# Kernel tuning notes

Measured on AMD Instinct MI355X. Metric: run time of the kernel, lower is better.

Reference implementation:

```python
import jax, jax.numpy as jnp
import numpy as np

B, S = 4, 128
N_ITERS = 3  # original hardcodes range(3) regardless of max_iter


def _build_masks(edge_mask, chart_mask):
    S_ = edge_mask.shape[-1]
    ar = jnp.arange(S_)
    ne = ar[:, None] != ar[None, :]          # [a,b]: a != b
    le = ar[:, None] <= ar[None, :]
    ge = ar[:, None] >= ar[None, :]
    ls = jnp.minimum(ar[:, None], ar[None, :])  # min(a,b)
    rs = jnp.maximum(ar[:, None], ar[None, :])  # max(a,b)

    # edge_mask2o[b,h,m,s] = edge_mask[b,h,s] & edge_mask[b,h,m] & (m != s)
    em2o = edge_mask[:, :, None, :] & edge_mask[:, :, :, None]
    em2o = em2o & ne[None, None, :, :]
    # lrhs[h,m,s] = (min(m,s) >= h) | (max(m,s) <= h)
    lrhs = (ls[None, :, :] >= ar[:, None, None]) | (rs[None, :, :] <= ar[:, None, None])
    noncross = em2o & lrhs[None]
    # additionally require h != s for plain edge_mask2o
    em2o = em2o & ne[:, None, :][None]

    cm0 = chart_mask[:, 0]                                  # [B,S]
    pad = cm0[:, :, None] & cm0[:, None, :]                 # [B,S,S]
    chart_r = jnp.roll(chart_mask, 1, axis=1)               # cat((cm[:,-1:], cm[:,:-1]))
    # span_mask2o[b,i,j,s] = chart_r[b,i,j] & pad[b,j,s] & (max(i,j) != s)
    span2o = chart_r[:, :, :, None] & pad[:, None, :, :]
    span2o = span2o & (rs[:, :, None] != ar[None, None, :])[None]
    # inside[i,j,s] = (i <= s) & (j >= s)
    inside = le[:, None, :] & ge[None, :, :]
    outside = (~inside)[None] & span2o
    # off-diagonal pad mask: pad.triu(1) | pad.tril(-1) == pad & (i != j)
    outside = outside & (pad & ne[None])[:, :, :, None]
    return em2o, noncross, span2o, outside


def setup_inputs() -> dict:
    key = jax.random.key(0)
    ks = jax.random.split(key, 12)
    lens = jax.random.randint(ks[0], (B,), S // 2, S)
    valid = jnp.arange(S)[None, :] < lens[:, None]          # [B,S]
    edge_mask = valid[:, :, None] & valid[:, None, :]
    tri = jnp.triu(jnp.ones((S, S), dtype=bool), 1)
    chart_mask = edge_mask & tri[None]
    def rn(k, shape):
        return jax.random.normal(k, shape, dtype=jnp.float32)
    return {
        's_edge': rn(ks[1], (B, S, S)),
        's_const': rn(ks[2], (B, S, S)),
        's_sib': rn(ks[3], (B, S, S, S)),
        's_cop': rn(ks[4], (B, S, S, S)),
        's_grd': rn(ks[5], (B, S, S, S)),
        's_end_point': rn(ks[6], (B, S, S, S)),
        's_split': rn(ks[7], (B, S, S, S)),
        's_head_span_b': rn(ks[8], (B, S, S, S)),
        's_head_span_e': rn(ks[9], (B, S, S, S)),
        'edge_mask': edge_mask,
        'chart_mask': chart_mask,
    }


def reference(s_edge, s_const, s_sib, s_cop, s_grd, s_end_point, s_split,
              s_head_span_b, s_head_span_e, edge_mask, chart_mask):
    # symmetrize span scores: triu + triu(1).T on last two dims
    s_span = jnp.triu(s_const) + jnp.swapaxes(jnp.triu(s_const, 1), -1, -2)
    em2o, noncross, span2o, outside = _build_masks(edge_mask, chart_mask)

    s_sib = s_sib * em2o
    s_cop = s_cop * em2o
    s_grd = s_grd * em2o
    s_end_point = s_end_point * noncross
    s_split = s_split * span2o
    s_hb = s_head_span_b * outside
    s_he = jnp.transpose(s_head_span_e, (0, 2, 1, 3)) * outside

    # Note: the torch code aliases tmp_q_edge to s_edge and uses +=, so the
    # base scores accumulate across iterations; equivalently q <- q + update.
    q_edge, q_span = s_edge, s_span
    for _ in range(N_ITERS):
        pe = jax.nn.sigmoid(q_edge)
        ps = jax.nn.sigmoid(q_span)
        upd_e = (jnp.einsum('bhs,bhms->bhm', pe, s_sib)
                 + jnp.einsum('bsm,bhms->bhm', pe, s_cop)
                 + jnp.einsum('bms,bhms->bhm', ps, s_grd)
                 + jnp.einsum('bms,bhms->bhm', ps, s_end_point))
        upd_s = (jnp.einsum('bis,bijs->bis', ps, s_split)
                 + jnp.einsum('bsi,bijs->bij', pe, s_hb)
                 + jnp.einsum('bsj,bijs->bij', pe, s_he))
        q_edge = q_edge + upd_e
        q_span = q_span + upd_s
    return q_edge, q_span
```

## Files before the change

### kernel.cpp

```cpp
#include <hip/hip_runtime.h>
#include <stdint.h>

#define BB 4
#define SDIM 128
#define S2 (SDIM*SDIM)
#define S3 ((size_t)SDIM*S2)

__device__ __forceinline__ int probe_len(const void* em, int b, int lane) {
    const unsigned char* p8 = (const unsigned char*)em;
    const int* p32 = (const int*)em;
    const int t0 = lane, t1 = lane + 64;
    const size_t i0 = (size_t)b*S2 + (size_t)t0*SDIM + t0;
    const size_t i1 = (size_t)b*S2 + (size_t)t1*SDIM + t1;
    const unsigned char a0 = p8[i0], a1 = p8[i1];
    const bool ok = (a0 != 0) && (t1 != SDIM-1 || a1 == 0);
    const unsigned long long mok = __ballot(ok);
    const bool use8 = (mok == ~0ull);
    int v0, v1;
    if (use8) { v0 = (a0 != 0); v1 = (a1 != 0); }
    else      { v0 = (p32[i0] != 0); v1 = (p32[i1] != 0); }
    return __popcll(__ballot(v0)) + __popcll(__ballot(v1));
}

__device__ __forceinline__ float sigf(float x) { return 1.f / (1.f + expf(-x)); }

__device__ __forceinline__ void gll16(const float* g, float* l) {
    __builtin_amdgcn_global_load_lds(
        (const __attribute__((address_space(1))) void*)g,
        (__attribute__((address_space(3))) void*)l, 16, 0, 0);
}

__global__ __launch_bounds__(256) void k_prep(
    const float* __restrict__ s_edge, const float* __restrict__ s_const,
    const float* __restrict__ s_split, const void* __restrict__ em,
    float* __restrict__ q_edge, float* __restrict__ q_span,
    float* __restrict__ split0, float* __restrict__ split1,
    float* __restrict__ peA, float* __restrict__ peB,
    float* __restrict__ peTA, float* __restrict__ peTB,
    float* __restrict__ psA, float* __restrict__ psB) {
    __shared__ float plds[64*SDIM];
    __shared__ float red2[2][SDIM];
    const int b = blockIdx.x >> 7, i = blockIdx.x & 127;
    const int y = blockIdx.y;
    const int tid = threadIdx.x, lane = tid & 63, wave = tid >> 6;
    const int len = probe_len(em, b, lane);
    const int lm1 = len - 1;
    const size_t vb = (size_t)b*S2;
    if (y == 0 && tid < SDIM) {
        const size_t ro = vb + (size_t)i*SDIM + tid;
        const float qe = s_edge[ro];
        const float qs = (i <= tid) ? s_const[ro] : s_const[vb + (size_t)tid*SDIM + i];
        q_edge[ro] = qe;
        q_span[ro] = qs;
        const float se = sigf(qe), ss = sigf(qs);
        peA[ro] = se; peB[ro] = se;
        psA[ro] = ss; psB[ro] = ss;
        const size_t to = vb + (size_t)tid*SDIM + i;
        peTA[to] = se; peTB[to] = se;
    }
    if (i >= 1 && i < len) {
        const int L = len - i;
        const float* sb = s_split + (size_t)b*S3 + (size_t)i*S2;
        for (int mloc = wave; mloc < 32; mloc += 4) {
            const int t0 = 2*(y + 2*mloc);
            if (t0 >= L) break;
            const int j = i + t0 + (lane >> 5);
            const int jc = min(j, lm1);
            gll16(sb + (size_t)jc*SDIM + (lane & 31)*4, &plds[(2*mloc)*SDIM]);
        }
    }
    __syncthreads();
    const int k = tid & 127, rh = tid >> 7;
    float sum = 0.f;
    #pragma unroll
    for (int u = 0; u < 32; ++u) {
        const int r = rh + 2*u;
        const int j = i + 4*u + 2*y + rh;
        sum += (j < len && j != k) ? plds[r*SDIM + k] : 0.f;
    }
    red2[rh][k] = sum;
    __syncthreads();
    if (tid < SDIM) {
        float* out = y ? split1 : split0;
        out[vb + (size_t)i*SDIM + tid] =
            (i >= 1 && i < len && tid >= 1 && tid < len)
            ? (red2[0][tid] + red2[1][tid]) : 0.f;
    }
}

__global__ __launch_bounds__(256) void k_upd(
    const float* __restrict__ s_sib, const float* __restrict__ s_cop,
    const float* __restrict__ s_grd, const float* __restrict__ s_ep,
    const float* __restrict__ s_hb,  const float* __restrict__ s_he,
    const float* __restrict__ peA, const float* __restrict__ peTA,
    const float* __restrict__ psA,
    const float* __restrict__ split0, const float* __restrict__ split1,
    const void* __restrict__ em,
    float* __restrict__ q_edge, float* __restrict__ q_span,
    float* __restrict__ peB, float* __restrict__ peTB, float* __restrict__ psB) {
    __shared__ float lds[6*16*SDIM];
    __shared__ float sml[64];
    const int b = blockIdx.x >> 7, row = blockIdx.x & 127;
    const int tid = threadIdx.x, wave = tid >> 6, lane = tid & 63;
    const int half = lane >> 5, sq = (lane & 31) * 4;
    const int len = probe_len(em, b, lane);
    const int lm1 = len - 1;
    const size_t vb = (size_t)b*S2;

    if (blockIdx.y < 8) {
        const int h = row;
        const int m0 = blockIdx.y * 16;
        if (h >= len || m0 >= len) return;
        const size_t tb = (size_t)b*S3 + (size_t)h*S2;
        const size_t hrow = vb + (size_t)h*SDIM;
        const float* bases[6] = { s_sib + tb, s_cop + tb, s_grd + tb,
                                  s_ep + tb,  peTA + vb,  psA + vb };
        #pragma unroll
        for (int T = 0; T < 6; ++T) {
            #pragma unroll
            for (int ss = 0; ss < 2; ++ss) {
                const int s  = 2*wave + ss;
                const int r2 = 2*s + half;
                const int mc = min(m0 + r2, lm1);
                gll16(bases[T] + (size_t)mc*SDIM + sq, &lds[(T*16 + 2*s)*SDIM]);
            }
        }
        if (tid < 16)
            sml[tid] = q_edge[hrow + min(m0 + tid, lm1)];
        __syncthreads();
        const float4 pe4 = *(const float4*)(peA + hrow + sq);
        #pragma unroll
        for (int it = 0; it < 2; ++it) {
            const int m = m0 + it*8 + wave*2 + half;
            const int r = it*8 + wave*2 + half;
            const float4 sibv = *(const float4*)&lds[(0*16 + r)*SDIM + sq];
            const float4 copv = *(const float4*)&lds[(1*16 + r)*SDIM + sq];
            const float4 grdv = *(const float4*)&lds[(2*16 + r)*SDIM + sq];
            const float4 epvv = *(const float4*)&lds[(3*16 + r)*SDIM + sq];
            const float4 petv = *(const float4*)&lds[(4*16 + r)*SDIM + sq];
            const float4 psvv = *(const float4*)&lds[(5*16 + r)*SDIM + sq];
            const bool mv = (m < len);
            float rr = 0.f;
            #define TERM(C, F) { const int s = sq + C;                               \
                const bool bs = mv && (s < len) && (m != s);                         \
                const float fem = (bs && (h != s)) ? 1.f : 0.f;                      \
                const float fnc = (bs && ((m >= h && s >= h) || (m <= h && s <= h))) \
                                  ? 1.f : 0.f;                                       \
                rr += fem * (sibv.F*pe4.F + copv.F*petv.F + grdv.F*psvv.F)           \
                    + fnc * (epvv.F*psvv.F); }
            TERM(0, x) TERM(1, y) TERM(2, z) TERM(3, w)
            #undef TERM
            rr += __shfl_xor(rr, 16); rr += __shfl_xor(rr, 8); rr += __shfl_xor(rr, 4);
            rr += __shfl_xor(rr, 2);  rr += __shfl_xor(rr, 1);
            if ((lane & 31) == 0 && mv) {
                const float qn = sml[r] + rr;
                q_edge[hrow + m] = qn;
                const float sg = sigf(qn);
                peB[hrow + m] = sg;
                peTB[vb + (size_t)m*SDIM + h] = sg;
            }
        }
    } else {
        const int i = row;
        const int j0 = (blockIdx.y - 8) * 16;
        if (i < 1 || i >= len || j0 >= len) return;
        const size_t irow = vb + (size_t)i*SDIM;
        #pragma unroll
        for (int ss = 0; ss < 2; ++ss) {
            const int s  = 2*wave + ss;
            const int r2 = 2*s + half;
            const int jc = min(j0 + r2, lm1);
            gll16(s_hb + (size_t)b*S3 + (size_t)i*S2 + (size_t)jc*SDIM + sq,
                  &lds[(0*16 + 2*s)*SDIM]);
            gll16(s_he + (size_t)b*S3 + (size_t)jc*S2 + (size_t)i*SDIM + sq,
                  &lds[(1*16 + 2*s)*SDIM]);
            gll16(peTA + vb + (size_t)jc*SDIM + sq,
                  &lds[(2*16 + 2*s)*SDIM]);
        }
        if (tid < 64) {
            const int surf = tid >> 4, jj = tid & 15;
            const int jc = min(j0 + jj, lm1);
            const size_t o = irow + jc;
            const float v = (surf == 0) ? q_span[o]
                          : (surf == 1) ? psA[o]
                          : (surf == 2) ? split0[o] : split1[o];
            sml[tid] = v;
        }
        __syncthreads();
        const float4 peTi4 = *(const float4*)(peTA + irow + sq);
        #pragma unroll
        for (int it = 0; it < 2; ++it) {
            const int j = j0 + it*8 + wave*2 + half;
            const int r = it*8 + wave*2 + half;
            const float4 hbv  = *(const float4*)&lds[(0*16 + r)*SDIM + sq];
            const float4 hev  = *(const float4*)&lds[(1*16 + r)*SDIM + sq];
            const float4 ptjv = *(const float4*)&lds[(2*16 + r)*SDIM + sq];
            const bool act = (j > i) && (j < len);
            float rr = 0.f;
            #define TERM(C, F) { const int s = sq + C;                               \
                const float f = (act && s >= 1 && s < len && (s < i || s > j))       \
                                ? 1.f : 0.f;                                         \
                rr += f * (hbv.F*peTi4.F + hev.F*ptjv.F); }
            TERM(0, x) TERM(1, y) TERM(2, z) TERM(3, w)
            #undef TERM
            rr += __shfl_xor(rr, 16); rr += __shfl_xor(rr, 8); rr += __shfl_xor(rr, 4);
            rr += __shfl_xor(rr, 2);  rr += __shfl_xor(rr, 1);
            if ((lane & 31) == 0 && j >= 1 && j < len) {
                const float qn = sml[r] + rr + sml[16 + r] * (sml[32 + r] + sml[48 + r]);
                q_span[irow + j] = qn;
                psB[irow + j] = sigf(qn);
            }
        }
    }
}

extern "C" void kernel_launch(void* const* d_in, const int* in_sizes, int n_in,
                              void* d_out, int out_size, void* d_ws, size_t ws_size,
                              hipStream_t stream) {
    const float* s_edge  = (const float*)d_in[0];
    const float* s_const = (const float*)d_in[1];
    const float* s_sib   = (const float*)d_in[2];
    const float* s_cop   = (const float*)d_in[3];
    const float* s_grd   = (const float*)d_in[4];
    const float* s_ep    = (const float*)d_in[5];
    const float* s_split = (const float*)d_in[6];
    const float* s_hb    = (const float*)d_in[7];
    const float* s_he    = (const float*)d_in[8];
    const void*  em      = d_in[9];
    (void)in_sizes; (void)n_in; (void)out_size; (void)ws_size;

    float* q_edge = (float*)d_out;
    float* q_span = q_edge + (size_t)BB * S2;

    char* ws = (char*)d_ws;
    const size_t SZ = (size_t)BB * S2 * sizeof(float);
    float* split0 = (float*)(ws);
    float* split1 = (float*)(ws + 1*SZ);
    float* peA    = (float*)(ws + 2*SZ);
    float* peTA   = (float*)(ws + 3*SZ);
    float* psA    = (float*)(ws + 4*SZ);
    float* peB    = (float*)(ws + 5*SZ);
    float* peTB   = (float*)(ws + 6*SZ);
    float* psB    = (float*)(ws + 7*SZ);

    const int NB = BB * SDIM;
    hipLaunchKernelGGL(k_prep, dim3(NB, 2), dim3(256), 0, stream,
                       s_edge, s_const, s_split, em, q_edge, q_span,
                       split0, split1, peA, peB, peTA, peTB, psA, psB);
    for (int it = 0; it < 3; ++it) {
        const int s = it & 1;
        const float* peR  = s ? peB  : peA;
        const float* peTR = s ? peTB : peTA;
        const float* psR  = s ? psB  : psA;
        float* peW  = s ? peA  : peB;
        float* peTW = s ? peTA : peTB;
        float* psW  = s ? psA  : psB;
        hipLaunchKernelGGL(k_upd, dim3(dim3(NB, 16)), dim3(256), 0, stream,
                           s_sib, s_cop, s_grd, s_ep, s_hb, s_he,
                           peR, peTR, psR, split0, split1, em,
                           q_edge, q_span, peW, peTW, psW);
    }
}
```

Baseline: 294.6 us.

## Restructure update kernels into per-row persistent blocks with double-buffered async loads

The grid changes from many 16-row tiles per (batch,row) to one block per row and part. Each block loops over 8-row chunks and double-buffers global-to-LDS loads, using explicit vmcnt waits so the next chunk's fetch overlaps compute on the current one. The split prep kernel is collapsed into a single pass that writes one summed split buffer, and span rows below the diagonal skip the tensor loads entirely. This trades grid-level parallelism (fewer, longer blocks) for less redundant row-header loading and better latency hiding, with the risk of lower occupancy and load imbalance across rows of different lengths.

```diff
diff --git a/kernel.cpp b/kernel.cpp
--- a/kernel.cpp
+++ b/kernel.cpp
@@ -34,19 +34,18 @@
     const float* __restrict__ s_edge, const float* __restrict__ s_const,
     const float* __restrict__ s_split, const void* __restrict__ em,
     float* __restrict__ q_edge, float* __restrict__ q_span,
-    float* __restrict__ split0, float* __restrict__ split1,
+    float* __restrict__ splitsum,
     float* __restrict__ peA, float* __restrict__ peB,
     float* __restrict__ peTA, float* __restrict__ peTB,
     float* __restrict__ psA, float* __restrict__ psB) {
-    __shared__ float plds[64*SDIM];
-    __shared__ float red2[2][SDIM];
+    __shared__ float pbuf[2][8][SDIM];
+    __shared__ float pred[2][SDIM];
     const int b = blockIdx.x >> 7, i = blockIdx.x & 127;
-    const int y = blockIdx.y;
-    const int tid = threadIdx.x, lane = tid & 63, wave = tid >> 6;
+    const int tid = threadIdx.x, lane = tid & 63, wave = tid >> 6, half = lane >> 5;
     const int len = probe_len(em, b, lane);
     const int lm1 = len - 1;
     const size_t vb = (size_t)b*S2;
-    if (y == 0 && tid < SDIM) {
+    if (tid < SDIM) {
         const size_t ro = vb + (size_t)i*SDIM + tid;
         const float qe = s_edge[ro];
         const float qs = (i <= tid) ? s_const[ro] : s_const[vb + (size_t)tid*SDIM + i];
@@ -58,34 +57,42 @@
         const size_t to = vb + (size_t)tid*SDIM + i;
         peTA[to] = se; peTB[to] = se;
     }
+    float sumv = 0.f;
     if (i >= 1 && i < len) {
-        const int L = len - i;
         const float* sb = s_split + (size_t)b*S3 + (size_t)i*S2;
-        for (int mloc = wave; mloc < 32; mloc += 4) {
-            const int t0 = 2*(y + 2*mloc);
-            if (t0 >= L) break;
-            const int j = i + t0 + (lane >> 5);
-            const int jc = min(j, lm1);
-            gll16(sb + (size_t)jc*SDIM + (lane & 31)*4, &plds[(2*mloc)*SDIM]);
-        }
-    }
-    __syncthreads();
-    const int k = tid & 127, rh = tid >> 7;
-    float sum = 0.f;
-    #pragma unroll
-    for (int u = 0; u < 32; ++u) {
-        const int r = rh + 2*u;
-        const int j = i + 4*u + 2*y + rh;
-        sum += (j < len && j != k) ? plds[r*SDIM + k] : 0.f;
-    }
-    red2[rh][k] = sum;
-    __syncthreads();
-    if (tid < SDIM) {
-        float* out = y ? split1 : split0;
-        out[vb + (size_t)i*SDIM + tid] =
-            (i >= 1 && i < len && tid >= 1 && tid < len)
-            ? (red2[0][tid] + red2[1][tid]) : 0.f;
-    }
+        const int sq = (lane & 31) * 4;
+        const int nc = (len - i + 7) >> 3;
+        #define PSTAGE(CB, C) { \
+            const int jc_ = min(i + 8*(C) + 2*wave + half, lm1); \
+            gll16(sb + (size_t)jc_*SDIM + sq, &pbuf[CB][2*wave][0]); }
+        PSTAGE(0, 0)
+        const int k = tid & 127, rh = tid >> 7;
+        float acc = 0.f;
+        for (int c = 0; c < nc; ++c) {
+            const int cb = c & 1;
+            if (c + 1 < nc) {
+                PSTAGE(cb ^ 1, c + 1)
+                asm volatile("s_waitcnt vmcnt(1)" ::: "memory");
+            } else {
+                asm volatile("s_waitcnt vmcnt(0)" ::: "memory");
+            }
+            __builtin_amdgcn_s_barrier();
+            #pragma unroll
+            for (int rr2 = 0; rr2 < 4; ++rr2) {
+                const int r = rh*4 + rr2;
+                const int j = i + 8*c + r;
+                const float v = pbuf[cb][r][k];
+                acc += (j < len && j != k) ? v : 0.f;
+            }
+            __builtin_amdgcn_s_barrier();
+        }
+        #undef PSTAGE
+        pred[rh][k] = acc;
+        __syncthreads();
+        if (tid >= 1 && tid < len && tid < SDIM)
+            sumv = pred[0][tid] + pred[1][tid];
+    }
+    if (tid < SDIM) splitsum[vb + (size_t)i*SDIM + tid] = sumv;
 }
 
 __global__ __launch_bounds__(256) void k_upd(
@@ -93,53 +100,57 @@
     const float* __restrict__ s_grd, const float* __restrict__ s_ep,
     const float* __restrict__ s_hb,  const float* __restrict__ s_he,
     const float* __restrict__ peA, const float* __restrict__ peTA,
-    const float* __restrict__ psA,
-    const float* __restrict__ split0, const float* __restrict__ split1,
+    const float* __restrict__ psA, const float* __restrict__ splitsum,
     const void* __restrict__ em,
     float* __restrict__ q_edge, float* __restrict__ q_span,
     float* __restrict__ peB, float* __restrict__ peTB, float* __restrict__ psB) {
-    __shared__ float lds[6*16*SDIM];
-    __shared__ float sml[64];
-    const int b = blockIdx.x >> 7, row = blockIdx.x & 127;
+    __shared__ float buf[2][6][8][SDIM];
+    __shared__ float sml[3*SDIM];
+    const int gid = blockIdx.x;
+    const int part = gid & 1, b = (gid >> 1) & 3, row = gid >> 3;
     const int tid = threadIdx.x, wave = tid >> 6, lane = tid & 63;
     const int half = lane >> 5, sq = (lane & 31) * 4;
     const int len = probe_len(em, b, lane);
     const int lm1 = len - 1;
     const size_t vb = (size_t)b*S2;
 
-    if (blockIdx.y < 8) {
+    if (part == 0) {
         const int h = row;
-        const int m0 = blockIdx.y * 16;
-        if (h >= len || m0 >= len) return;
+        if (h >= len) return;
         const size_t tb = (size_t)b*S3 + (size_t)h*S2;
         const size_t hrow = vb + (size_t)h*SDIM;
-        const float* bases[6] = { s_sib + tb, s_cop + tb, s_grd + tb,
-                                  s_ep + tb,  peTA + vb,  psA + vb };
-        #pragma unroll
-        for (int T = 0; T < 6; ++T) {
-            #pragma unroll
-            for (int ss = 0; ss < 2; ++ss) {
-                const int s  = 2*wave + ss;
-                const int r2 = 2*s + half;
-                const int mc = min(m0 + r2, lm1);
-                gll16(bases[T] + (size_t)mc*SDIM + sq, &lds[(T*16 + 2*s)*SDIM]);
-            }
-        }
-        if (tid < 16)
-            sml[tid] = q_edge[hrow + min(m0 + tid, lm1)];
+        const float4 pe4 = *(const float4*)(peA + hrow + sq);
+        if (tid < SDIM) sml[tid] = q_edge[hrow + tid];
         __syncthreads();
-        const float4 pe4 = *(const float4*)(peA + hrow + sq);
-        #pragma unroll
-        for (int it = 0; it < 2; ++it) {
-            const int m = m0 + it*8 + wave*2 + half;
-            const int r = it*8 + wave*2 + half;
-            const float4 sibv = *(const float4*)&lds[(0*16 + r)*SDIM + sq];
-            const float4 copv = *(const float4*)&lds[(1*16 + r)*SDIM + sq];
-            const float4 grdv = *(const float4*)&lds[(2*16 + r)*SDIM + sq];
-            const float4 epvv = *(const float4*)&lds[(3*16 + r)*SDIM + sq];
-            const float4 petv = *(const float4*)&lds[(4*16 + r)*SDIM + sq];
-            const float4 psvv = *(const float4*)&lds[(5*16 + r)*SDIM + sq];
+        const int nc = (len + 7) >> 3;
+        #define ESTAGE(CB, C) { \
+            const int mc_ = min(8*(C) + 2*wave + half, lm1); \
+            const size_t go = (size_t)mc_*SDIM + sq; \
+            gll16(s_sib + tb + go, &buf[CB][0][2*wave][0]); \
+            gll16(s_cop + tb + go, &buf[CB][1][2*wave][0]); \
+            gll16(s_grd + tb + go, &buf[CB][2][2*wave][0]); \
+            gll16(s_ep  + tb + go, &buf[CB][3][2*wave][0]); \
+            gll16(peTA + vb + go, &buf[CB][4][2*wave][0]); \
+            gll16(psA  + vb + go, &buf[CB][5][2*wave][0]); }
+        ESTAGE(0, 0)
+        for (int c = 0; c < nc; ++c) {
+            const int cb = c & 1;
+            if (c + 1 < nc) {
+                ESTAGE(cb ^ 1, c + 1)
+                asm volatile("s_waitcnt vmcnt(6)" ::: "memory");
+            } else {
+                asm volatile("s_waitcnt vmcnt(0)" ::: "memory");
+            }
+            __builtin_amdgcn_s_barrier();
+            const int r = 2*wave + half;
+            const int m = 8*c + r;
             const bool mv = (m < len);
+            const float4 sibv = *(const float4*)&buf[cb][0][r][sq];
+            const float4 copv = *(const float4*)&buf[cb][1][r][sq];
+            const float4 grdv = *(const float4*)&buf[cb][2][r][sq];
+            const float4 epvv = *(const float4*)&buf[cb][3][r][sq];
+            const float4 petv = *(const float4*)&buf[cb][4][r][sq];
+            const float4 psvv = *(const float4*)&buf[cb][5][r][sq];
             float rr = 0.f;
             #define TERM(C, F) { const int s = sq + C;                               \
                 const bool bs = mv && (s < len) && (m != s);                         \
@@ -153,63 +164,76 @@
             rr += __shfl_xor(rr, 16); rr += __shfl_xor(rr, 8); rr += __shfl_xor(rr, 4);
             rr += __shfl_xor(rr, 2);  rr += __shfl_xor(rr, 1);
             if ((lane & 31) == 0 && mv) {
-                const float qn = sml[r] + rr;
+                const float qn = sml[m] + rr;
                 q_edge[hrow + m] = qn;
                 const float sg = sigf(qn);
                 peB[hrow + m] = sg;
                 peTB[vb + (size_t)m*SDIM + h] = sg;
             }
-        }
+            __builtin_amdgcn_s_barrier();
+        }
+        #undef ESTAGE
     } else {
         const int i = row;
-        const int j0 = (blockIdx.y - 8) * 16;
-        if (i < 1 || i >= len || j0 >= len) return;
+        if (i < 1 || i >= len) return;
         const size_t irow = vb + (size_t)i*SDIM;
-        #pragma unroll
-        for (int ss = 0; ss < 2; ++ss) {
-            const int s  = 2*wave + ss;
-            const int r2 = 2*s + half;
-            const int jc = min(j0 + r2, lm1);
-            gll16(s_hb + (size_t)b*S3 + (size_t)i*S2 + (size_t)jc*SDIM + sq,
-                  &lds[(0*16 + 2*s)*SDIM]);
-            gll16(s_he + (size_t)b*S3 + (size_t)jc*S2 + (size_t)i*SDIM + sq,
-                  &lds[(1*16 + 2*s)*SDIM]);
-            gll16(peTA + vb + (size_t)jc*SDIM + sq,
-                  &lds[(2*16 + 2*s)*SDIM]);
-        }
-        if (tid < 64) {
-            const int surf = tid >> 4, jj = tid & 15;
-            const int jc = min(j0 + jj, lm1);
-            const size_t o = irow + jc;
-            const float v = (surf == 0) ? q_span[o]
-                          : (surf == 1) ? psA[o]
-                          : (surf == 2) ? split0[o] : split1[o];
-            sml[tid] = v;
+        const size_t ibase = (size_t)b*S3 + (size_t)i*S2;
+        const float4 peTi4 = *(const float4*)(peTA + irow + sq);
+        for (int u = tid; u < 3*SDIM; u += 256) {
+            const int surf = u >> 7, t2 = u & 127;
+            sml[u] = (surf == 0) ? q_span[irow + t2]
+                   : (surf == 1) ? psA[irow + t2] : splitsum[irow + t2];
         }
         __syncthreads();
-        const float4 peTi4 = *(const float4*)(peTA + irow + sq);
-        #pragma unroll
-        for (int it = 0; it < 2; ++it) {
-            const int j = j0 + it*8 + wave*2 + half;
-            const int r = it*8 + wave*2 + half;
-            const float4 hbv  = *(const float4*)&lds[(0*16 + r)*SDIM + sq];
-            const float4 hev  = *(const float4*)&lds[(1*16 + r)*SDIM + sq];
-            const float4 ptjv = *(const float4*)&lds[(2*16 + r)*SDIM + sq];
-            const bool act = (j > i) && (j < len);
-            float rr = 0.f;
-            #define TERM(C, F) { const int s = sq + C;                               \
-                const float f = (act && s >= 1 && s < len && (s < i || s > j))       \
-                                ? 1.f : 0.f;                                         \
-                rr += f * (hbv.F*peTi4.F + hev.F*ptjv.F); }
-            TERM(0, x) TERM(1, y) TERM(2, z) TERM(3, w)
-            #undef TERM
-            rr += __shfl_xor(rr, 16); rr += __shfl_xor(rr, 8); rr += __shfl_xor(rr, 4);
-            rr += __shfl_xor(rr, 2);  rr += __shfl_xor(rr, 1);
-            if ((lane & 31) == 0 && j >= 1 && j < len) {
-                const float qn = sml[r] + rr + sml[16 + r] * (sml[32 + r] + sml[48 + r]);
-                q_span[irow + j] = qn;
-                psB[irow + j] = sigf(qn);
-            }
+        const int c0 = (i + 1) >> 3;
+        const int nc = (len + 7) >> 3;
+        for (int j2 = tid; j2 < 8*c0; j2 += 256) {
+            if (j2 >= 1) {
+                const float qn = sml[j2] + sml[SDIM + j2] * sml[2*SDIM + j2];
+                q_span[irow + j2] = qn;
+                psB[irow + j2] = sigf(qn);
+            }
+        }
+        if (c0 < nc) {
+            #define SSTAGE(CB, C) { \
+                const int jc_ = min(8*(C) + 2*wave + half, lm1); \
+                gll16(s_hb + ibase + (size_t)jc_*SDIM + sq, &buf[CB][0][2*wave][0]); \
+                gll16(s_he + (size_t)b*S3 + (size_t)jc_*S2 + (size_t)i*SDIM + sq, \
+                      &buf[CB][1][2*wave][0]); \
+                gll16(peTA + vb + (size_t)jc_*SDIM + sq, &buf[CB][2][2*wave][0]); }
+            SSTAGE(0, c0)
+            for (int c = c0; c < nc; ++c) {
+                const int cb = (c - c0) & 1;
+                if (c + 1 < nc) {
+                    SSTAGE(cb ^ 1, c + 1)
+                    asm volatile("s_waitcnt vmcnt(3)" ::: "memory");
+                } else {
+                    asm volatile("s_waitcnt vmcnt(0)" ::: "memory");
+                }
+                __builtin_amdgcn_s_barrier();
+                const int r = 2*wave + half;
+                const int j = 8*c + r;
+                const bool act = (j > i) && (j < len);
+                const float4 hbv  = *(const float4*)&buf[cb][0][r][sq];
+                const float4 hev  = *(const float4*)&buf[cb][1][r][sq];
+                const float4 ptjv = *(const float4*)&buf[cb][2][r][sq];
+                float rr = 0.f;
+                #define TERM(C, F) { const int s = sq + C;                           \
+                    const float f = (act && s >= 1 && s < len && (s < i || s > j))   \
+                                    ? 1.f : 0.f;                                     \
+                    rr += f * (hbv.F*peTi4.F + hev.F*ptjv.F); }
+                TERM(0, x) TERM(1, y) TERM(2, z) TERM(3, w)
+                #undef TERM
+                rr += __shfl_xor(rr, 16); rr += __shfl_xor(rr, 8); rr += __shfl_xor(rr, 4);
+                rr += __shfl_xor(rr, 2);  rr += __shfl_xor(rr, 1);
+                if ((lane & 31) == 0 && j >= 1 && j < len) {
+                    const float qn = sml[j] + rr + sml[SDIM + j] * sml[2*SDIM + j];
+                    q_span[irow + j] = qn;
+                    psB[irow + j] = sigf(qn);
+                }
+                __builtin_amdgcn_s_barrier();
+            }
+            #undef SSTAGE
         }
     }
 }
@@ -234,19 +258,18 @@
 
     char* ws = (char*)d_ws;
     const size_t SZ = (size_t)BB * S2 * sizeof(float);
-    float* split0 = (float*)(ws);
-    float* split1 = (float*)(ws + 1*SZ);
-    float* peA    = (float*)(ws + 2*SZ);
-    float* peTA   = (float*)(ws + 3*SZ);
-    float* psA    = (float*)(ws + 4*SZ);
-    float* peB    = (float*)(ws + 5*SZ);
-    float* peTB   = (float*)(ws + 6*SZ);
-    float* psB    = (float*)(ws + 7*SZ);
+    float* splitsum = (float*)(ws);
+    float* peA    = (float*)(ws + 1*SZ);
+    float* peTA   = (float*)(ws + 2*SZ);
+    float* psA    = (float*)(ws + 3*SZ);
+    float* peB    = (float*)(ws + 4*SZ);
+    float* peTB   = (float*)(ws + 5*SZ);
+    float* psB    = (float*)(ws + 6*SZ);
 
     const int NB = BB * SDIM;
-    hipLaunchKernelGGL(k_prep, dim3(NB, 2), dim3(256), 0, stream,
+    hipLaunchKernelGGL(k_prep, dim3(NB), dim3(256), 0, stream,
                        s_edge, s_const, s_split, em, q_edge, q_span,
-                       split0, split1, peA, peB, peTA, peTB, psA, psB);
+                       splitsum, peA, peB, peTA, peTB, psA, psB);
     for (int it = 0; it < 3; ++it) {
         const int s = it & 1;
         const float* peR  = s ? peB  : peA;
@@ -255,9 +278,9 @@
         float* peW  = s ? peA  : peB;
         float* peTW = s ? peTA : peTB;
         float* psW  = s ? psA  : psB;
-        hipLaunchKernelGGL(k_upd, dim3(dim3(NB, 16)), dim3(256), 0, stream,
+        hipLaunchKernelGGL(k_upd, dim3(2*NB), dim3(256), 0, stream,
                            s_sib, s_cop, s_grd, s_ep, s_hb, s_he,
-                           peR, peTR, psR, split0, split1, em,
+                           peR, peTR, psR, splitsum, em,
                            q_edge, q_span, peW, peTW, psW);
     }
 }
```

New measurement: 339.2 us. 1.15x slower.
